# Optimization experiments

Hardware: AMD Instinct MI355X
Metric: run time of the kernel (lower is better)

## Reference

```python
import jax, jax.numpy as jnp
import numpy as np

H = 8          # heads
F = 256        # hidden dim (hid_dim_1 == hid_dim_2)
D = F // H     # per-head dim = 32
NE = 3         # num edge types
NT = 2         # num node types: 0=op, 1=var
N = 50000      # nodes per type
E = 150000     # edges per edge type
F3 = 128       # hid_dim_3 = hid_dim_2 // 2
C = 16         # out_channels
ETYPES = [(0, 1), (1, 0), (0, 0)]  # (src_type, dst_type) per edge type
SQRT_D = float(np.sqrt(D))


def gelu(x):
    return jax.nn.gelu(x, approximate=False)  # torch F.gelu default (erf)


def layer_norm(x, g, b):
    mu = jnp.mean(x, -1, keepdims=True)
    var = jnp.mean((x - mu) ** 2, -1, keepdims=True)
    return (x - mu) * jax.lax.rsqrt(var + 1e-5) * g + b


def segment_softmax(a, seg, num_segments):
    # PyG softmax: subtract per-segment max, add 1e-16 to denominator
    m = jax.ops.segment_max(a, seg, num_segments=num_segments)
    m = jnp.where(jnp.isfinite(m), m, 0.0)
    e = jnp.exp(a - m[seg])
    s = jax.ops.segment_sum(e, seg, num_segments=num_segments)
    return e / (s[seg] + 1e-16)


def hgt_conv(xs, eis, Wkqv, bkqv, Wkrel, Wvrel, prel, Wout, bout, skip):
    # fused per-node-type K/Q/V projection, split as torch.tensor_split(., 3, dim=1)
    kqv = [xs[t] @ Wkqv[t] + bkqv[t] for t in range(NT)]
    k = [a[:, :F].reshape(-1, H, D) for a in kqv]
    q = [a[:, F:2 * F].reshape(-1, H, D) for a in kqv]
    v = [a[:, 2 * F:].reshape(-1, H, D) for a in kqv]
    off = [0]
    for x in xs:
        off.append(off[-1] + x.shape[0])
    ntot = off[-1]
    alphas, vjs, dsts = [], [], []
    for e, (st, dt) in enumerate(ETYPES):
        # per-(head, edge-type) relation transforms of source K/V (k_rel / v_rel)
        ke = jnp.einsum('nhd,hde->nhe', k[st], Wkrel[:, e])
        ve = jnp.einsum('nhd,hde->nhe', v[st], Wvrel[:, e])
        src, dst = eis[e][0], eis[e][1]
        a = jnp.sum(q[dt][dst] * ke[src], -1) * prel[e] / SQRT_D  # [E, H]
        alphas.append(a)
        vjs.append(ve[src])
        dsts.append(dst + off[dt])
    seg = jnp.concatenate(dsts, 0)
    # softmax over ALL incoming edges of a dst node across edge types (bipartite union)
    a = segment_softmax(jnp.concatenate(alphas, 0), seg, ntot)
    agg = jax.ops.segment_sum(jnp.concatenate(vjs, 0) * a[:, :, None], seg,
                              num_segments=ntot).reshape(ntot, F)
    outs = []
    for t in range(NT):
        o = gelu(agg[off[t]:off[t + 1]]) @ Wout[t] + bout[t]
        s = jax.nn.sigmoid(skip[t])
        outs.append(s * o + (1.0 - s) * xs[t])  # in==out -> skip gate active
    return outs


def _forward(x_op, x_var,
             l1_Wkqv, l1_bkqv, l1_Wkrel, l1_Wvrel, l1_prel, l1_Wout, l1_bout, l1_skip,
             l2_Wkqv, l2_bkqv, l2_Wkrel, l2_Wvrel, l2_prel, l2_Wout, l2_bout, l2_skip,
             l3_Wkqv, l3_bkqv, l3_Wkrel, l3_Wvrel, l3_prel, l3_Wout, l3_bout, l3_skip,
             ln_g, ln_b, Wagg1, bagg1, Wagg2, bagg2, Wo, bo,
             ei_ov, ei_vo, ei_oo):
    xs = [x_op, x_var]
    eis = [ei_ov, ei_vo, ei_oo]
    h = hgt_conv(xs, eis, l1_Wkqv, l1_bkqv, l1_Wkrel, l1_Wvrel, l1_prel, l1_Wout, l1_bout, l1_skip)
    h = [gelu(layer_norm(h[t], ln_g[t], ln_b[t])) for t in range(NT)]  # dropout = identity (eval)
    h = hgt_conv(h, eis, l2_Wkqv, l2_bkqv, l2_Wkrel, l2_Wvrel, l2_prel, l2_Wout, l2_bout, l2_skip)
    h = [gelu(x) for x in h]
    h = hgt_conv(h, eis, l3_Wkqv, l3_bkqv, l3_Wkrel, l3_Wvrel, l3_prel, l3_Wout, l3_bout, l3_skip)
    h = [gelu(x) for x in h]
    # HeteroLinear lin_agg_1 with type_vec = node type id (sorted by construction)
    ha = jnp.concatenate([h[0] @ Wagg1[0] + bagg1[0],
                          h[1] @ Wagg1[1] + bagg1[1]], 0)
    ha = jnp.mean(gelu(ha), 0)          # mean over all nodes -> [F]
    ha = gelu(ha @ Wagg2 + bagg2)       # [F3]
    return jnp.nan_to_num(ha @ Wo + bo) # [C]


def setup_inputs():
    key = jax.random.key(0)
    ks = jax.random.split(key, 64)
    it = iter(range(64))
    def nrm(shape, scale=0.05):
        return jax.random.normal(ks[next(it)], shape, dtype=jnp.float32) * scale
    inp = {
        'x_op': nrm((N, F), 1.0),
        'x_var': nrm((N, F), 1.0),
    }
    for i in (1, 2, 3):
        inp[f'l{i}_Wkqv'] = nrm((NT, F, 3 * F))
        inp[f'l{i}_bkqv'] = jnp.zeros((NT, 3 * F), jnp.float32)
        inp[f'l{i}_Wkrel'] = nrm((H, NE, D, D), 0.15)
        inp[f'l{i}_Wvrel'] = nrm((H, NE, D, D), 0.15)
        inp[f'l{i}_prel'] = jnp.ones((NE, H), jnp.float32)
        inp[f'l{i}_Wout'] = nrm((NT, F, F))
        inp[f'l{i}_bout'] = jnp.zeros((NT, F), jnp.float32)
        inp[f'l{i}_skip'] = jnp.ones((NT,), jnp.float32)
    inp['ln_g'] = jnp.ones((NT, F), jnp.float32)
    inp['ln_b'] = jnp.zeros((NT, F), jnp.float32)
    inp['Wagg1'] = nrm((NE, F, F))
    inp['bagg1'] = jnp.zeros((NE, F), jnp.float32)
    inp['Wagg2'] = nrm((F, F3))
    inp['bagg2'] = jnp.zeros((F3,), jnp.float32)
    inp['Wo'] = nrm((F3, C))
    inp['bo'] = jnp.zeros((C,), jnp.float32)
    ek = jax.random.split(jax.random.key(1), 3)
    inp['ei_ov'] = jax.random.randint(ek[0], (2, E), 0, N, dtype=jnp.int32)
    inp['ei_vo'] = jax.random.randint(ek[1], (2, E), 0, N, dtype=jnp.int32)
    inp['ei_oo'] = jax.random.randint(ek[2], (2, E), 0, N, dtype=jnp.int32)
    return inp


def reference(x_op, x_var,
              l1_Wkqv, l1_bkqv, l1_Wkrel, l1_Wvrel, l1_prel, l1_Wout, l1_bout, l1_skip,
              l2_Wkqv, l2_bkqv, l2_Wkrel, l2_Wvrel, l2_prel, l2_Wout, l2_bout, l2_skip,
              l3_Wkqv, l3_bkqv, l3_Wkrel, l3_Wvrel, l3_prel, l3_Wout, l3_bout, l3_skip,
              ln_g, ln_b, Wagg1, bagg1, Wagg2, bagg2, Wo, bo,
              ei_ov, ei_vo, ei_oo):
    return _forward(x_op, x_var,
                    l1_Wkqv, l1_bkqv, l1_Wkrel, l1_Wvrel, l1_prel, l1_Wout, l1_bout, l1_skip,
                    l2_Wkqv, l2_bkqv, l2_Wkrel, l2_Wvrel, l2_prel, l2_Wout, l2_bout, l2_skip,
                    l3_Wkqv, l3_bkqv, l3_Wkrel, l3_Wvrel, l3_prel, l3_Wout, l3_bout, l3_skip,
                    ln_g, ln_b, Wagg1, bagg1, Wagg2, bagg2, Wo, bo,
                    ei_ov, ei_vo, ei_oo)
```

## Files before the change

### kernel.cpp

```cpp
#include <hip/hip_runtime.h>
#include <math.h>

#define NN   50000
#define NTOT 100000
#define FD   256
#define EC   150000

static const size_t NF = (size_t)NN * FD;

typedef __attribute__((ext_vector_type(8))) short bf16x8;
typedef __attribute__((ext_vector_type(4))) float f32x4;

__device__ __forceinline__ float gelu_f(float x) {
  return 0.5f * x * (1.0f + erff(x * 0.7071067811865475f));
}
__device__ __forceinline__ unsigned short f2bf(float x) {
  unsigned u = __float_as_uint(x);
  u += 0x7FFFu + ((u >> 16) & 1u);
  return (unsigned short)(u >> 16);
}
__device__ __forceinline__ float bf2f(unsigned short u) {
  return __uint_as_float((unsigned)u << 16);
}

template<int MODE, int XSF>
__global__ __launch_bounds__(256) void gemm_bf(
    const unsigned short* __restrict__ A,
    const unsigned short* __restrict__ Bt,
    const float* __restrict__ bias,
    void* d0, void* d1, void* d2,
    const void* Xs, const float* __restrict__ skipp, int M)
{
  __shared__ unsigned short As[128 * 64];
  __shared__ unsigned short Bs[128 * 64];
  const int tid = threadIdx.x;
  const int lane = tid & 63;
  const int wave = tid >> 6;
  const int wr = wave >> 1, wc = wave & 1;
  const int l15 = lane & 15, lq = lane >> 4;
  const int bm = blockIdx.y * 128, bn = blockIdx.x * 128;
  const int sr = tid >> 1, sg0 = (tid & 1) * 4;
  const bool av = (bm + sr) < M;
  const unsigned short* ag = A  + (size_t)(bm + sr) * 256 + sg0 * 8;
  const unsigned short* bg = Bt + (size_t)(bn + sr) * 256 + sg0 * 8;

  f32x4 acc[4][4] = {};
  uint4 ra[4], rb[4];

#define LOADT(KT) { \
    const unsigned short* ap = ag + (KT) * 64; \
    const unsigned short* bp = bg + (KT) * 64; \
    if (av) { ra[0] = *(const uint4*)(ap);      ra[1] = *(const uint4*)(ap + 8); \
              ra[2] = *(const uint4*)(ap + 16); ra[3] = *(const uint4*)(ap + 24); } \
    else    { ra[0] = ra[1] = ra[2] = ra[3] = make_uint4(0,0,0,0); } \
    rb[0] = *(const uint4*)(bp);      rb[1] = *(const uint4*)(bp + 8); \
    rb[2] = *(const uint4*)(bp + 16); rb[3] = *(const uint4*)(bp + 24); }

  LOADT(0);
  for (int kt = 0; kt < 4; kt++) {
    __syncthreads();
    #pragma unroll
    for (int i = 0; i < 4; i++) {
      const int g = sg0 + i;
      *(uint4*)&As[sr * 64 + ((g ^ (sr & 7)) << 3)] = ra[i];
      *(uint4*)&Bs[sr * 64 + ((g ^ (sr & 7)) << 3)] = rb[i];
    }
    __syncthreads();
    if (kt < 3) LOADT(kt + 1);
    #pragma unroll
    for (int ks = 0; ks < 2; ks++) {
      bf16x8 af[4], bv[4];
      const int g = ks * 4 + lq;
      #pragma unroll
      for (int mi = 0; mi < 4; mi++) {
        const int r = wr * 64 + mi * 16 + l15;
        af[mi] = *(const bf16x8*)&As[r * 64 + ((g ^ (r & 7)) << 3)];
      }
      #pragma unroll
      for (int ni = 0; ni < 4; ni++) {
        const int c = wc * 64 + ni * 16 + l15;
        bv[ni] = *(const bf16x8*)&Bs[c * 64 + ((g ^ (c & 7)) << 3)];
      }
      #pragma unroll
      for (int mi = 0; mi < 4; mi++)
        #pragma unroll
        for (int ni = 0; ni < 4; ni++)
          acc[mi][ni] = __builtin_amdgcn_mfma_f32_16x16x32_bf16(
              af[mi], bv[ni], acc[mi][ni], 0, 0, 0);
    }
  }
#undef LOADT

  const int seg = (MODE == 0 || MODE == 3) ? (bn >> 8) : 0;
  float sg = 0.f;
  if (MODE == 1) sg = 1.f / (1.f + expf(-skipp[0]));
  #pragma unroll
  for (int mi = 0; mi < 4; mi++) {
    #pragma unroll
    for (int ni = 0; ni < 4; ni++) {
      const int cp = bn + wc * 64 + ni * 16 + l15;
      const float bc_ = bias[cp];
      const int co = (MODE == 0 || MODE == 3) ? (cp & 255) : cp;
      #pragma unroll
      for (int j = 0; j < 4; j++) {
        const int r = bm + wr * 64 + mi * 16 + lq * 4 + j;
        if (r >= M) continue;
        float v = acc[mi][ni][j] + bc_;
        const size_t oidx = (size_t)r * 256 + co;
        if (MODE == 2) {
          ((float*)d0)[oidx] = gelu_f(v);
        } else if (MODE == 1) {
          const float xs = XSF ? bf2f(((const unsigned short*)Xs)[oidx])
                               : ((const float*)Xs)[oidx];
          ((unsigned short*)d0)[oidx] = f2bf(sg * v + (1.f - sg) * xs);
        } else if (MODE == 0) {
          if (seg == 0) ((float*)d0)[oidx] = v;
          else ((unsigned short*)(seg == 1 ? d1 : d2))[oidx] = f2bf(v);
        } else {
          ((unsigned short*)(seg == 0 ? d0 : d1))[oidx] = f2bf(v);
        }
      }
    }
  }
}

__global__ __launch_bounds__(256) void wcomb_kernel(
    const float* __restrict__ Wkqv, const float* __restrict__ bkqv,
    const float* __restrict__ Wkrel, const float* __restrict__ Wvrel,
    const float* __restrict__ prel,
    unsigned short* __restrict__ Bo1t, unsigned short* __restrict__ Bvt,
    unsigned short* __restrict__ Bo3t,
    float* __restrict__ bias_o1, float* __restrict__ bias_v, float* __restrict__ bias_o3)
{
  const int z = blockIdx.x, et = z >> 1, kv = z & 1;
  const int h = blockIdx.y;
  const int st = (et == 1) ? 1 : 0;
  const int cbase = (kv ? 512 : 0) + h * 32;
  const float scale = kv ? 1.0f : (prel[et*8 + h] * 0.1767766952966369f);
  unsigned short* Bdst; int ofs; float* bdst;
  if (z == 0)      { Bdst = Bo1t; ofs = 0;   bdst = bias_o1; }
  else if (z == 1) { Bdst = Bo1t; ofs = 256; bdst = bias_o1; }
  else if (z == 2) { Bdst = Bvt;  ofs = 256; bdst = bias_v;  }
  else if (z == 3) { Bdst = Bvt;  ofs = 512; bdst = bias_v;  }
  else if (z == 4) { Bdst = Bo3t; ofs = 256; bdst = bias_o3; }
  else             { Bdst = Bo3t; ofs = 512; bdst = bias_o3; }
  __shared__ float Wr[32][32];
  const int tid = threadIdx.x;
  {
    const float* wr = (kv ? Wvrel : Wkrel) + ((size_t)(h*3 + et)) * 1024;
    for (int i = tid; i < 1024; i += 256) Wr[i >> 5][i & 31] = wr[i];
  }
  __syncthreads();
  const float* w1 = Wkqv + (size_t)st * 196608 + (size_t)tid * 768 + cbase;
  float acc[32] = {};
  for (int d = 0; d < 32; d++) {
    float v = w1[d];
    #pragma unroll
    for (int j = 0; j < 32; j++) acc[j] = fmaf(v, Wr[d][j], acc[j]);
  }
  for (int j = 0; j < 32; j++)
    Bdst[(size_t)(ofs + h * 32 + j) * 256 + tid] = f2bf(acc[j] * scale);
  if (tid < 32) {
    const float* bk = bkqv + st * 768 + cbase;
    float a = 0.f;
    for (int d = 0; d < 32; d++) a = fmaf(bk[d], Wr[d][tid], a);
    bdst[ofs + h * 32 + tid] = a * scale;
  }
}

__global__ __launch_bounds__(256) void qpack_kernel(
    const float* __restrict__ Wkqv, const float* __restrict__ bkqv,
    unsigned short* __restrict__ Bo3t, unsigned short* __restrict__ Bvt,
    float* __restrict__ bias_o3, float* __restrict__ bias_v)
{
  const int r = blockIdx.x, t = blockIdx.y, c = threadIdx.x;
  float w = Wkqv[(size_t)t * 196608 + (size_t)r * 768 + 256 + c];
  (t ? Bvt : Bo3t)[(size_t)c * 256 + r] = f2bf(w);
  if (r == 0) (t ? bias_v : bias_o3)[c] = bkqv[t * 768 + 256 + c];
}

__global__ __launch_bounds__(256) void wcvt_kernel(
    const float* __restrict__ src, unsigned short* __restrict__ dst)
{
  const int r = blockIdx.x, c = threadIdx.x;
  dst[(size_t)c * 256 + r] = f2bf(src[(size_t)r * 256 + c]);
}

__global__ __launch_bounds__(256) void attn_union(
    const float* __restrict__ qb,
    const unsigned short* __restrict__ KEu,
    const unsigned short* __restrict__ VEu,
    const int* __restrict__ indptr, const int* __restrict__ adj,
    unsigned short* __restrict__ aggb)
{
  const int wid = (int)(((size_t)blockIdx.x * 256 + threadIdx.x) >> 6);
  if (wid >= NN) return;
  const int lane = threadIdx.x & 63;
  const int off = lane * 4;
  const float4 q4 = *(const float4*)(qb + (size_t)wid * FD + off);
  float m = -INFINITY, s = 0.f, ax = 0.f, ay = 0.f, az = 0.f, aw = 0.f;
  const int beg = indptr[wid], end = indptr[wid + 1];
  for (int i = beg; i < end; i++) {
    const int src = adj[i];
    ushort4 ku = *(const ushort4*)(KEu + (size_t)src * FD + off);
    float d = q4.x*bf2f(ku.x) + q4.y*bf2f(ku.y) + q4.z*bf2f(ku.z) + q4.w*bf2f(ku.w);
    d += __shfl_xor(d, 1); d += __shfl_xor(d, 2); d += __shfl_xor(d, 4);
    float mn = fmaxf(m, d);
    float sc = expf(m - mn);
    float w  = expf(d - mn);
    s = s * sc + w;
    ushort4 vu = *(const ushort4*)(VEu + (size_t)src * FD + off);
    ax = ax*sc + w*bf2f(vu.x); ay = ay*sc + w*bf2f(vu.y);
    az = az*sc + w*bf2f(vu.z); aw = aw*sc + w*bf2f(vu.w);
    m = mn;
  }
  const float inv = 1.f / (s + 1e-16f);
  ushort4 o;
  o.x = f2bf(gelu_f(ax * inv)); o.y = f2bf(gelu_f(ay * inv));
  o.z = f2bf(gelu_f(az * inv)); o.w = f2bf(gelu_f(aw * inv));
  *(ushort4*)(aggb + (size_t)wid * FD + off) = o;
}

__global__ __launch_bounds__(256) void ln_gelu_kernel(
    unsigned short* __restrict__ x, const float* __restrict__ g,
    const float* __restrict__ b)
{
  const int wid = (int)(((size_t)blockIdx.x * 256 + threadIdx.x) >> 6);
  if (wid >= NTOT) return;
  const int lane = threadIdx.x & 63;
  const int t = (wid >= NN) ? 1 : 0;
  ushort4 u = *(ushort4*)(x + (size_t)wid * FD + lane*4);
  float vx = bf2f(u.x), vy = bf2f(u.y), vz = bf2f(u.z), vw = bf2f(u.w);
  float sum = vx + vy + vz + vw;
  #pragma unroll
  for (int o = 1; o < 64; o <<= 1) sum += __shfl_xor(sum, o);
  float mu = sum * (1.f/256.f);
  float dx = vx-mu, dy = vy-mu, dz = vz-mu, dw = vw-mu;
  float vs = dx*dx + dy*dy + dz*dz + dw*dw;
  #pragma unroll
  for (int o = 1; o < 64; o <<= 1) vs += __shfl_xor(vs, o);
  float var = vs * (1.f/256.f);
  float rs = 1.f / sqrtf(var + 1e-5f);
  int c = lane*4;
  float4 gv = *(const float4*)(g + t*FD + c);
  float4 bv = *(const float4*)(b + t*FD + c);
  ushort4 o4;
  o4.x = f2bf(gelu_f(dx*rs*gv.x + bv.x));
  o4.y = f2bf(gelu_f(dy*rs*gv.y + bv.y));
  o4.z = f2bf(gelu_f(dz*rs*gv.z + bv.z));
  o4.w = f2bf(gelu_f(dw*rs*gv.w + bv.w));
  *(ushort4*)(x + (size_t)wid * FD + c) = o4;
}

__global__ __launch_bounds__(256) void gelu_bf_kernel(
    unsigned short* __restrict__ x, size_t n4)
{
  size_t i = ((size_t)blockIdx.x * 256 + threadIdx.x);
  if (i >= n4) return;
  ushort4 u = ((ushort4*)x)[i];
  u.x = f2bf(gelu_f(bf2f(u.x))); u.y = f2bf(gelu_f(bf2f(u.y)));
  u.z = f2bf(gelu_f(bf2f(u.z))); u.w = f2bf(gelu_f(bf2f(u.w)));
  ((ushort4*)x)[i] = u;
}

__global__ __launch_bounds__(256) void cvt_bf_kernel(
    const float* __restrict__ src, unsigned short* __restrict__ dst, size_t n4)
{
  size_t i = ((size_t)blockIdx.x * 256 + threadIdx.x);
  if (i >= n4) return;
  float4 v = ((const float4*)src)[i];
  ushort4 o; o.x = f2bf(v.x); o.y = f2bf(v.y); o.z = f2bf(v.z); o.w = f2bf(v.w);
  ((ushort4*)dst)[i] = o;
}

__global__ __launch_bounds__(256) void count_v(const int* __restrict__ e0,
                                               int* __restrict__ degv) {
  int i = blockIdx.x * 256 + threadIdx.x;
  if (i >= EC) return;
  atomicAdd(&degv[e0[EC + i]], 1);
}
__global__ __launch_bounds__(256) void count_o(const int* __restrict__ e1,
                                               const int* __restrict__ e2,
                                               int* __restrict__ dego) {
  int i = blockIdx.x * 256 + threadIdx.x;
  if (i >= 2*EC) return;
  int dst = (i < EC) ? e1[EC + i] : e2[EC + (i - EC)];
  atomicAdd(&dego[dst], 1);
}
__global__ __launch_bounds__(1024) void scan_n(
    const int* __restrict__ deg, int* __restrict__ indptr,
    int* __restrict__ cursor, int n)
{
  __shared__ int ts[1024];
  const int tid = threadIdx.x;
  const int per = (n + 1023) / 1024;
  int s0 = tid * per, s1 = s0 + per; if (s1 > n) s1 = n; if (s0 > n) s0 = n;
  int loc = 0;
  for (int i = s0; i < s1; i++) loc += deg[i];
  ts[tid] = loc;
  __syncthreads();
  for (int off = 1; off < 1024; off <<= 1) {
    int v = (tid >= off) ? ts[tid - off] : 0;
    __syncthreads();
    ts[tid] += v;
    __syncthreads();
  }
  int base = (tid == 0) ? 0 : ts[tid - 1];
  for (int i = s0; i < s1; i++) {
    indptr[i] = base; cursor[i] = base; base += deg[i];
  }
  if (tid == 0) indptr[n] = ts[1023];
}
__global__ __launch_bounds__(256) void scat_v(const int* __restrict__ e0,
                                              int* __restrict__ cv,
                                              int* __restrict__ adjv) {
  int i = blockIdx.x * 256 + threadIdx.x;
  if (i >= EC) return;
  int pos = atomicAdd(&cv[e0[EC + i]], 1);
  adjv[pos] = e0[i];
}
__global__ __launch_bounds__(256) void scat_o(const int* __restrict__ e1,
                                              const int* __restrict__ e2,
                                              int* __restrict__ co,
                                              int* __restrict__ adjo) {
  int i = blockIdx.x * 256 + threadIdx.x;
  if (i >= 2*EC) return;
  int dst, srcg;
  if (i < EC) { dst = e1[EC + i]; srcg = NN + e1[i]; }
  else        { int j = i - EC; dst = e2[EC + j]; srcg = e2[j]; }
  int pos = atomicAdd(&co[dst], 1);
  adjo[pos] = srcg;
}

__global__ __launch_bounds__(256) void colmean_kernel(
    const float* __restrict__ gmat, double* __restrict__ outp, int n)
{
  const int c = threadIdx.x;
  const int r0 = blockIdx.x * 256;
  int rend = r0 + 256; if (rend > n) rend = n;
  double sum = 0.0;
  for (int r = r0; r < rend; r++) sum += (double)gmat[(size_t)r * FD + c];
  atomicAdd(&outp[c], sum);
}

__global__ __launch_bounds__(256) void head_kernel(
    const double* __restrict__ meand,
    const float* __restrict__ Wagg2, const float* __restrict__ bagg2,
    const float* __restrict__ Wo, const float* __restrict__ bo,
    float* __restrict__ outp)
{
  __shared__ float mv[256];
  __shared__ float h2[128];
  const int tid = threadIdx.x;
  mv[tid] = (float)(meand[tid] * (1.0 / (double)NTOT));
  __syncthreads();
  if (tid < 128) {
    float acc = bagg2[tid];
    for (int k = 0; k < 256; k++) acc = fmaf(mv[k], Wagg2[k*128 + tid], acc);
    h2[tid] = gelu_f(acc);
  }
  __syncthreads();
  if (tid < 16) {
    float acc = bo[tid];
    for (int k = 0; k < 128; k++) acc = fmaf(h2[k], Wo[k*16 + tid], acc);
    if (isnan(acc)) acc = 0.f;
    else if (isinf(acc)) acc = (acc > 0.f) ? 3.4028234663852886e38f : -3.4028234663852886e38f;
    outp[tid] = acc;
  }
}

__global__ void fill_kernel(float* p, int n, float v) {
  int i = blockIdx.x * 64 + threadIdx.x;
  if (i < n) p[i] = v;
}

extern "C" void kernel_launch(void* const* d_in, const int* in_sizes, int n_in,
                              void* d_out, int out_size, void* d_ws, size_t ws_size,
                              hipStream_t stream)
{
  const float* x_op_in  = (const float*)d_in[0];
  const float* x_var_in = (const float*)d_in[1];
  struct LayerP { const float *Wkqv,*bkqv,*Wkrel,*Wvrel,*prel,*Wout,*bout,*skip; };
  LayerP L[3];
  for (int i = 0; i < 3; i++) {
    int b = 2 + i*8;
    L[i].Wkqv  = (const float*)d_in[b+0];
    L[i].bkqv  = (const float*)d_in[b+1];
    L[i].Wkrel = (const float*)d_in[b+2];
    L[i].Wvrel = (const float*)d_in[b+3];
    L[i].prel  = (const float*)d_in[b+4];
    L[i].Wout  = (const float*)d_in[b+5];
    L[i].bout  = (const float*)d_in[b+6];
    L[i].skip  = (const float*)d_in[b+7];
  }
  const float* ln_g  = (const float*)d_in[26];
  const float* ln_b  = (const float*)d_in[27];
  const float* Wagg1 = (const float*)d_in[28];
  const float* bagg1 = (const float*)d_in[29];
  const float* Wagg2 = (const float*)d_in[30];
  const float* bagg2 = (const float*)d_in[31];
  const float* Wo    = (const float*)d_in[32];
  const float* bo    = (const float*)d_in[33];
  const int* e0 = (const int*)d_in[34];
  const int* e1 = (const int*)d_in[35];
  const int* e2 = (const int*)d_in[36];

  float* base = (float*)d_ws;
  unsigned short* Xb   = (unsigned short*)base;
  unsigned short* Xbop = Xb;
  unsigned short* Xbvar= Xb + NF;
  float* Qb            = base + NF;
  unsigned short* aggb = (unsigned short*)(base + 2*NF);
  unsigned short* KEu  = (unsigned short*)(base + 2*NF + NF/2);
  unsigned short* VEu  = (unsigned short*)(base + 3*NF + NF/2);
  float* wb            = base + 4*NF + NF/2;
  unsigned short* Bo1t = (unsigned short*)wb;
  unsigned short* Bvt  = Bo1t + 512*256;
  unsigned short* Bo3t = Bvt + 768*256;
  unsigned short* Wtt  = Bo3t + 768*256;
  float* b_o1 = (float*)(Wtt + 8*65536);
  float* b_v  = b_o1 + 512;
  float* b_o3 = b_v + 768;
  double* meand = (double*)(b_o3 + 768);
  int* ipv  = (int*)(meand + 256);
  int* ipo  = ipv + (NN + 1);
  int* cv   = ipo + (NN + 1);
  int* co   = cv + NN;
  int* degv = co + NN;
  int* dego = degv + NN;
  int* adjv = dego + NN;
  int* adjo = adjv + EC;
  size_t need = (size_t)((char*)(adjo + 2*EC) - (char*)d_ws);
  if (ws_size < need) {
    float v = (float)(ws_size >> 20) * 1000.0f;
    fill_kernel<<<dim3((out_size + 63)/64), 64, 0, stream>>>((float*)d_out, out_size, v);
    return;
  }

  hipMemsetAsync(degv, 0, 2*NN*sizeof(int), stream);
  hipMemsetAsync(meand, 0, 256*sizeof(double), stream);
  count_v<<<dim3((EC + 255)/256), 256, 0, stream>>>(e0, degv);
  count_o<<<dim3((2*EC + 255)/256), 256, 0, stream>>>(e1, e2, dego);
  scan_n<<<dim3(1), 1024, 0, stream>>>(degv, ipv, cv, NN);
  scan_n<<<dim3(1), 1024, 0, stream>>>(dego, ipo, co, NN);
  scat_v<<<dim3((EC + 255)/256), 256, 0, stream>>>(e0, cv, adjv);
  scat_o<<<dim3((2*EC + 255)/256), 256, 0, stream>>>(e1, e2, co, adjo);

  for (int i = 0; i < 3; i++) {
    wcvt_kernel<<<dim3(256), 256, 0, stream>>>(L[i].Wout,         Wtt + (size_t)(i*2)  *65536);
    wcvt_kernel<<<dim3(256), 256, 0, stream>>>(L[i].Wout + 65536, Wtt + (size_t)(i*2+1)*65536);
  }
  wcvt_kernel<<<dim3(256), 256, 0, stream>>>(Wagg1,         Wtt + (size_t)6*65536);
  wcvt_kernel<<<dim3(256), 256, 0, stream>>>(Wagg1 + 65536, Wtt + (size_t)7*65536);
  cvt_bf_kernel<<<dim3((int)(NF/4 + 255)/256), 256, 0, stream>>>(x_op_in,  Xbop,  NF/4);
  cvt_bf_kernel<<<dim3((int)(NF/4 + 255)/256), 256, 0, stream>>>(x_var_in, Xbvar, NF/4);

  const dim3 gw6(6, 391), gw4(4, 391), gw2(2, 391);
  const dim3 ga((NN*64 + 255)/256);

  for (int layer = 0; layer < 3; layer++) {
    const LayerP& P = L[layer];
    const unsigned short* Wo_op  = Wtt + (size_t)(layer*2)  *65536;
    const unsigned short* Wo_var = Wtt + (size_t)(layer*2+1)*65536;

    wcomb_kernel<<<dim3(6, 8), 256, 0, stream>>>(P.Wkqv, P.bkqv, P.Wkrel, P.Wvrel,
                                                 P.prel, Bo1t, Bvt, Bo3t, b_o1, b_v, b_o3);
    qpack_kernel<<<dim3(256, 2), 256, 0, stream>>>(P.Wkqv, P.bkqv, Bo3t, Bvt, b_o3, b_v);

    gemm_bf<3,0><<<gw4, 256, 0, stream>>>(
        Xbop, Bo1t, b_o1, KEu, VEu, nullptr, nullptr, nullptr, NN);
    gemm_bf<0,0><<<gw6, 256, 0, stream>>>(
        Xbvar, Bvt, b_v, Qb, KEu + NF, VEu + NF, nullptr, nullptr, NN);
    attn_union<<<ga, 256, 0, stream>>>(Qb, KEu, VEu, ipv, adjv, aggb);
    if (layer == 0)
      gemm_bf<1,0><<<gw2, 256, 0, stream>>>(aggb, Wo_var, P.bout + 256,
          Xbvar, nullptr, nullptr, x_var_in, P.skip + 1, NN);
    else
      gemm_bf<1,1><<<gw2, 256, 0, stream>>>(aggb, Wo_var, P.bout + 256,
          Xbvar, nullptr, nullptr, Xbvar, P.skip + 1, NN);

    gemm_bf<0,0><<<gw6, 256, 0, stream>>>(
        Xbop, Bo3t, b_o3, Qb, KEu, VEu, nullptr, nullptr, NN);
    attn_union<<<ga, 256, 0, stream>>>(Qb, KEu, VEu, ipo, adjo, aggb);
    if (layer == 0)
      gemm_bf<1,0><<<gw2, 256, 0, stream>>>(aggb, Wo_op, P.bout,
          Xbop, nullptr, nullptr, x_op_in, P.skip, NN);
    else
      gemm_bf<1,1><<<gw2, 256, 0, stream>>>(aggb, Wo_op, P.bout,
          Xbop, nullptr, nullptr, Xbop, P.skip, NN);

    if (layer == 0)
      ln_gelu_kernel<<<dim3((NTOT*64 + 255)/256), 256, 0, stream>>>(Xb, ln_g, ln_b);
    else
      gelu_bf_kernel<<<dim3((int)(2*NF/4 + 255)/256), 256, 0, stream>>>(Xb, 2*NF/4);
  }

  gemm_bf<2,0><<<gw2, 256, 0, stream>>>(Xbop, Wtt + (size_t)6*65536, bagg1,
      Qb, nullptr, nullptr, nullptr, nullptr, NN);
  colmean_kernel<<<dim3((NN + 255)/256), 256, 0, stream>>>(Qb, meand, NN);
  gemm_bf<2,0><<<gw2, 256, 0, stream>>>(Xbvar, Wtt + (size_t)7*65536, bagg1 + 256,
      Qb, nullptr, nullptr, nullptr, nullptr, NN);
  colmean_kernel<<<dim3((NN + 255)/256), 256, 0, stream>>>(Qb, meand, NN);
  head_kernel<<<dim3(1), 256, 0, stream>>>(meand, Wagg2, bagg2, Wo, bo, (float*)d_out);
}
```

Baseline: 2.304 ms.

## Parallelize CSR prefix scan across blocks and tile weight transposes through LDS

Replaces the two single-block 1024-thread prefix scans over 50k degrees with a three-pass multi-block scan (partial sums, tiny mid scan, finalize), run on both degree arrays in one launch. Separately, the weight transpose/convert kernels now stage 32x32 tiles in shared memory so both global reads and writes are coalesced. This removes serial setup latency in preprocessing, at the cost of two extra small launches and a fixed chunk count tied to NN. The end pointer is now set from the constant edge count instead of the computed sum.

```diff
diff --git a/kernel.cpp b/kernel.cpp
--- a/kernel.cpp
+++ b/kernel.cpp
@@ -5,6 +5,7 @@
 #define NTOT 100000
 #define FD   256
 #define EC   150000
+#define NCH  98
 
 static const size_t NF = (size_t)NN * FD;
 
@@ -173,17 +174,40 @@
     unsigned short* __restrict__ Bo3t, unsigned short* __restrict__ Bvt,
     float* __restrict__ bias_o3, float* __restrict__ bias_v)
 {
-  const int r = blockIdx.x, t = blockIdx.y, c = threadIdx.x;
-  float w = Wkqv[(size_t)t * 196608 + (size_t)r * 768 + 256 + c];
-  (t ? Bvt : Bo3t)[(size_t)c * 256 + r] = f2bf(w);
-  if (r == 0) (t ? bias_v : bias_o3)[c] = bkqv[t * 768 + 256 + c];
+  const int t = blockIdx.y;
+  const int bx = blockIdx.x & 7, by = blockIdx.x >> 3;
+  const int tx = threadIdx.x & 31, ty = threadIdx.x >> 5;
+  __shared__ float tile[32][33];
+  #pragma unroll
+  for (int k = 0; k < 4; k++) {
+    int r = by*32 + ty + 8*k, c = bx*32 + tx;
+    tile[ty + 8*k][tx] = Wkqv[(size_t)t*196608 + (size_t)r*768 + 256 + c];
+  }
+  __syncthreads();
+  unsigned short* dst = t ? Bvt : Bo3t;
+  #pragma unroll
+  for (int k = 0; k < 4; k++) {
+    int c = bx*32 + ty + 8*k, r = by*32 + tx;
+    dst[(size_t)c*256 + r] = f2bf(tile[tx][ty + 8*k]);
+  }
+  if (blockIdx.x == 0) {
+    (t ? bias_v : bias_o3)[threadIdx.x] = bkqv[t*768 + 256 + threadIdx.x];
+  }
 }
 
 __global__ __launch_bounds__(256) void wcvt_kernel(
     const float* __restrict__ src, unsigned short* __restrict__ dst)
 {
-  const int r = blockIdx.x, c = threadIdx.x;
-  dst[(size_t)c * 256 + r] = f2bf(src[(size_t)r * 256 + c]);
+  const int bx = blockIdx.x & 7, by = blockIdx.x >> 3;
+  const int tx = threadIdx.x & 31, ty = threadIdx.x >> 5;
+  __shared__ float tile[32][33];
+  #pragma unroll
+  for (int k = 0; k < 4; k++)
+    tile[ty + 8*k][tx] = src[(size_t)(by*32 + ty + 8*k)*256 + bx*32 + tx];
+  __syncthreads();
+  #pragma unroll
+  for (int k = 0; k < 4; k++)
+    dst[(size_t)(bx*32 + ty + 8*k)*256 + by*32 + tx] = f2bf(tile[tx][ty + 8*k]);
 }
 
 __global__ __launch_bounds__(256) void attn_union(
@@ -287,30 +311,68 @@
   int dst = (i < EC) ? e1[EC + i] : e2[EC + (i - EC)];
   atomicAdd(&dego[dst], 1);
 }
-__global__ __launch_bounds__(1024) void scan_n(
-    const int* __restrict__ deg, int* __restrict__ indptr,
-    int* __restrict__ cursor, int n)
-{
-  __shared__ int ts[1024];
+
+__global__ __launch_bounds__(256) void scan_part(
+    const int* __restrict__ deg,
+    int* __restrict__ psum)
+{
+  const int arr = blockIdx.y, ch = blockIdx.x, tid = threadIdx.x;
+  int i0 = ch*512 + tid, i1 = i0 + 256;
+  int s = ((i0 < NN) ? deg[arr*NN + i0] : 0) + ((i1 < NN) ? deg[arr*NN + i1] : 0);
+  __shared__ int red[256];
+  red[tid] = s; __syncthreads();
+  #pragma unroll
+  for (int off = 128; off > 0; off >>= 1) {
+    if (tid < off) red[tid] += red[tid + off];
+    __syncthreads();
+  }
+  if (tid == 0) psum[arr*NCH + ch] = red[0];
+}
+
+__global__ __launch_bounds__(256) void scan_mid(int* __restrict__ psum)
+{
   const int tid = threadIdx.x;
-  const int per = (n + 1023) / 1024;
-  int s0 = tid * per, s1 = s0 + per; if (s1 > n) s1 = n; if (s0 > n) s0 = n;
-  int loc = 0;
-  for (int i = s0; i < s1; i++) loc += deg[i];
-  ts[tid] = loc;
-  __syncthreads();
-  for (int off = 1; off < 1024; off <<= 1) {
-    int v = (tid >= off) ? ts[tid - off] : 0;
+  __shared__ int buf[2*NCH];
+  if (tid < 2*NCH) buf[tid] = psum[tid];
+  __syncthreads();
+  if (tid < 2) {
+    int run = 0;
+    for (int i = 0; i < NCH; i++) { int t = buf[tid*NCH + i]; buf[tid*NCH + i] = run; run += t; }
+  }
+  __syncthreads();
+  if (tid < 2*NCH) psum[tid] = buf[tid];
+}
+
+__global__ __launch_bounds__(256) void scan_fin(
+    const int* __restrict__ deg, const int* __restrict__ psum,
+    int* __restrict__ ipv, int* __restrict__ ipo,
+    int* __restrict__ cv, int* __restrict__ co)
+{
+  const int arr = blockIdx.y, ch = blockIdx.x, tid = threadIdx.x;
+  __shared__ int buf[512];
+  __shared__ int s2[256];
+  int i0 = ch*512 + 2*tid, i1 = i0 + 1;
+  buf[2*tid]   = (i0 < NN) ? deg[arr*NN + i0] : 0;
+  buf[2*tid+1] = (i1 < NN) ? deg[arr*NN + i1] : 0;
+  __syncthreads();
+  s2[tid] = buf[2*tid] + buf[2*tid+1];
+  __syncthreads();
+  #pragma unroll
+  for (int off = 1; off < 256; off <<= 1) {
+    int v = (tid >= off) ? s2[tid - off] : 0;
     __syncthreads();
-    ts[tid] += v;
+    s2[tid] += v;
     __syncthreads();
   }
-  int base = (tid == 0) ? 0 : ts[tid - 1];
-  for (int i = s0; i < s1; i++) {
-    indptr[i] = base; cursor[i] = base; base += deg[i];
-  }
-  if (tid == 0) indptr[n] = ts[1023];
-}
+  int ex = (tid ? s2[tid - 1] : 0) + psum[arr*NCH + ch];
+  int e0 = ex, e1 = ex + buf[2*tid];
+  int* ip  = arr ? ipo : ipv;
+  int* cur = arr ? co  : cv;
+  if (i0 < NN) { ip[i0] = e0; cur[i0] = e0; }
+  if (i1 < NN) { ip[i1] = e1; cur[i1] = e1; }
+  if (ch == 0 && tid == 0) ip[NN] = arr ? 2*EC : EC;
+}
+
 __global__ __launch_bounds__(256) void scat_v(const int* __restrict__ e0,
                                               int* __restrict__ cv,
                                               int* __restrict__ adjv) {
@@ -430,7 +492,8 @@
   int* dego = degv + NN;
   int* adjv = dego + NN;
   int* adjo = adjv + EC;
-  size_t need = (size_t)((char*)(adjo + 2*EC) - (char*)d_ws);
+  int* psum = adjo + 2*EC;
+  size_t need = (size_t)((char*)(psum + 2*NCH) - (char*)d_ws);
   if (ws_size < need) {
     float v = (float)(ws_size >> 20) * 1000.0f;
     fill_kernel<<<dim3((out_size + 63)/64), 64, 0, stream>>>((float*)d_out, out_size, v);
@@ -441,17 +504,18 @@
   hipMemsetAsync(meand, 0, 256*sizeof(double), stream);
   count_v<<<dim3((EC + 255)/256), 256, 0, stream>>>(e0, degv);
   count_o<<<dim3((2*EC + 255)/256), 256, 0, stream>>>(e1, e2, dego);
-  scan_n<<<dim3(1), 1024, 0, stream>>>(degv, ipv, cv, NN);
-  scan_n<<<dim3(1), 1024, 0, stream>>>(dego, ipo, co, NN);
+  scan_part<<<dim3(NCH, 2), 256, 0, stream>>>(degv, psum);
+  scan_mid<<<dim3(1), 256, 0, stream>>>(psum);
+  scan_fin<<<dim3(NCH, 2), 256, 0, stream>>>(degv, psum, ipv, ipo, cv, co);
   scat_v<<<dim3((EC + 255)/256), 256, 0, stream>>>(e0, cv, adjv);
   scat_o<<<dim3((2*EC + 255)/256), 256, 0, stream>>>(e1, e2, co, adjo);
 
   for (int i = 0; i < 3; i++) {
-    wcvt_kernel<<<dim3(256), 256, 0, stream>>>(L[i].Wout,         Wtt + (size_t)(i*2)  *65536);
-    wcvt_kernel<<<dim3(256), 256, 0, stream>>>(L[i].Wout + 65536, Wtt + (size_t)(i*2+1)*65536);
-  }
-  wcvt_kernel<<<dim3(256), 256, 0, stream>>>(Wagg1,         Wtt + (size_t)6*65536);
-  wcvt_kernel<<<dim3(256), 256, 0, stream>>>(Wagg1 + 65536, Wtt + (size_t)7*65536);
+    wcvt_kernel<<<dim3(64), 256, 0, stream>>>(L[i].Wout,         Wtt + (size_t)(i*2)  *65536);
+    wcvt_kernel<<<dim3(64), 256, 0, stream>>>(L[i].Wout + 65536, Wtt + (size_t)(i*2+1)*65536);
+  }
+  wcvt_kernel<<<dim3(64), 256, 0, stream>>>(Wagg1,         Wtt + (size_t)6*65536);
+  wcvt_kernel<<<dim3(64), 256, 0, stream>>>(Wagg1 + 65536, Wtt + (size_t)7*65536);
   cvt_bf_kernel<<<dim3((int)(NF/4 + 255)/256), 256, 0, stream>>>(x_op_in,  Xbop,  NF/4);
   cvt_bf_kernel<<<dim3((int)(NF/4 + 255)/256), 256, 0, stream>>>(x_var_in, Xbvar, NF/4);
 
@@ -465,7 +529,7 @@
 
     wcomb_kernel<<<dim3(6, 8), 256, 0, stream>>>(P.Wkqv, P.bkqv, P.Wkrel, P.Wvrel,
                                                  P.prel, Bo1t, Bvt, Bo3t, b_o1, b_v, b_o3);
-    qpack_kernel<<<dim3(256, 2), 256, 0, stream>>>(P.Wkqv, P.bkqv, Bo3t, Bvt, b_o3, b_v);
+    qpack_kernel<<<dim3(64, 2), 256, 0, stream>>>(P.Wkqv, P.bkqv, Bo3t, Bvt, b_o3, b_v);
 
     gemm_bf<3,0><<<gw4, 256, 0, stream>>>(
         Xbop, Bo1t, b_o1, KEu, VEu, nullptr, nullptr, nullptr, NN);
```

After: 2.097 ms. 1.1x faster.
